# Performance work log

Hardware: AMD Instinct MI355X
Metric: run time of the kernel (lower is better)

Reference implementation:

```python
import jax, jax.numpy as jnp
import numpy as np

N = 50000      # atoms
P = 1_600_000  # pairs
F = 128        # per-atom features
G = 16         # radial basis functions
H = 32         # vector features
HID1, HID2 = 256, 128
IN_F = 2 * F + 2 * H  # is_first_module=False: [rad_emb, vec_emb, rad_q, vec_q]


def setup_inputs() -> dict:
    key = jax.random.key(0)
    ks = jax.random.split(key, 13)
    return {
        "atomic_embedding": jax.random.normal(ks[0], (N, F), jnp.float32),
        "partial_charges": jax.random.normal(ks[1], (N, 1), jnp.float32),
        "pair_indices": jax.random.randint(ks[2], (2, P), 0, N),
        "gs": jax.random.uniform(ks[3], (P, G), jnp.float32),
        "gv": jax.random.normal(ks[4], (P, 3, G), jnp.float32),
        "agh": jax.random.normal(ks[5], (F, G, H), jnp.float32) * 0.05,
        "W_gf": jax.random.normal(ks[6], (G, F), jnp.float32) * 0.1,   # gs_to_fatom (no bias)
        "W1": jax.random.normal(ks[7], (IN_F, HID1), jnp.float32) * 0.05,
        "b1": jnp.zeros((HID1,), jnp.float32),
        "W2": jax.random.normal(ks[8], (HID1, HID2), jnp.float32) * 0.05,
        "b2": jnp.zeros((HID2,), jnp.float32),
        "W3": jax.random.normal(ks[9], (HID2, F + 2), jnp.float32) * 0.05,
        "b3": jnp.zeros((F + 2,), jnp.float32),
    }


def _safe_norm(x):
    # torch.norm has subgradient 0 at 0; avoid NaN grads for all-zero rows
    sq = jnp.sum(x * x, axis=-1)
    return jnp.sqrt(jnp.where(sq > 0, sq, 1.0)) * (sq > 0)


def _gelu(x):
    return jax.nn.gelu(x, approximate=False)  # torch nn.GELU default (erf)


def reference(atomic_embedding, partial_charges, pair_indices, gs, gv, agh,
              W_gf, W1, b1, W2, b2, W3, b3):
    idx_j = pair_indices[1]                       # (P,)
    a_j = atomic_embedding[idx_j]                 # (P, F) gather
    mapped_gs = gs @ W_gf                         # (P, F)

    # radial contributions from embeddings: scatter-add over pairs
    rad_emb = jnp.zeros((N, F), mapped_gs.dtype).at[idx_j].add(a_j * mapped_gs)

    # vector contributions: einsum contraction then scatter-add, then norm
    avf_v = jnp.einsum('pa,pdg,agh->phd', a_j, gv, agh)            # (P, H, 3)
    avf_sum = jnp.zeros((N, H, 3), avf_v.dtype).at[idx_j].add(avf_v)
    vec_emb = _safe_norm(avf_sum)                                   # (N, H)

    # charge branch (vector contributions skipped -> zeros)
    q_j = partial_charges[idx_j]                                    # (P, 1)
    rad_q = jnp.zeros((N, F), mapped_gs.dtype).at[idx_j].add(q_j * mapped_gs)
    vec_q = jnp.zeros((N, H), mapped_gs.dtype)

    msg = jnp.concatenate([rad_emb, vec_emb, rad_q, vec_q], axis=1)  # (N, IN_F)
    h = _gelu(msg @ W1 + b1)
    h = _gelu(h @ W2 + b2)
    out = h @ W3 + b3                                                # (N, F+2)

    delta_q, f, delta_a = out[:, :1], out[:, 1:2], out[:, 2:]
    return (delta_a, delta_q, f)
```

## Files before the change

kernel.cpp:

```cpp
#include <hip/hip_runtime.h>
#include <math.h>

#define N_ATOMS 50000
#define P_PAIRS 1600000
#define TA 16

__device__ __forceinline__ float gelu_exact(float x) {
    return 0.5f * x * (1.0f + erff(x * 0.70710678118654752440f));
}

__global__ __launch_bounds__(256) void scatter_kernel(
    const int* __restrict__ idx_j,
    const float* __restrict__ gs,
    const float* __restrict__ gv,
    float* __restrict__ acc)
{
    int t = blockIdx.x * 256 + threadIdx.x;
    int p = t >> 6;
    int c = t & 63;
    int idx = idx_j[p];
    float v = (c < 16) ? gs[p * 16 + c] : gv[p * 48 + (c - 16)];
    atomicAdd(acc + idx * 64 + c, v);
}

__global__ __launch_bounds__(256, 2) void fused_atom_kernel(
    const float* __restrict__ emb,
    const float* __restrict__ qch,
    const float* __restrict__ acc,
    const float* __restrict__ agh,
    const float* __restrict__ W_gf,
    const float* __restrict__ W1, const float* __restrict__ b1,
    const float* __restrict__ W2, const float* __restrict__ b2,
    const float* __restrict__ W3, const float* __restrict__ b3,
    float* __restrict__ out)
{
    __shared__ __align__(16) float s_bufA[16 * 256];
    __shared__ __align__(16) float s_bufB[16 * 512];
    __shared__ __align__(16) float s_msgT[320 * 16];
    __shared__ __align__(16) float s_gs[16 * 16];
    __shared__ __align__(16) float s_gv[16 * 48];
    __shared__ __align__(16) float s_q[16];

    const int tid = threadIdx.x;
    const int n0 = blockIdx.x * TA;

    float* s_embT = s_bufA;
    float* s_U    = s_bufB;
    float* s_h1T  = s_bufA;
    float* s_h2T  = s_bufB;

    #pragma unroll
    for (int i = 0; i < 2; i++) {
        int ii = tid + i * 256;
        int atom = ii >> 5;
        int a4 = (ii & 31) * 4;
        float4 v = *(const float4*)(emb + (size_t)(n0 + atom) * 128 + a4);
        s_embT[(a4 + 0) * 16 + atom] = v.x;
        s_embT[(a4 + 1) * 16 + atom] = v.y;
        s_embT[(a4 + 2) * 16 + atom] = v.z;
        s_embT[(a4 + 3) * 16 + atom] = v.w;
    }
    #pragma unroll
    for (int i = 0; i < 4; i++) {
        int ii = tid + i * 256;
        int atom = ii >> 6, c = ii & 63;
        float v = acc[(size_t)(n0 + atom) * 64 + c];
        if (c < 16) s_gs[atom * 16 + c] = v;
        else        s_gv[atom * 48 + (c - 16)] = v;
    }
    if (tid < 16) s_q[tid] = qch[n0 + tid];
    __syncthreads();

    {
        const int gh4  = (tid & 127) * 4;
        const int half = tid >> 7;
        float u[32];
        #pragma unroll
        for (int i = 0; i < 32; i++) u[i] = 0.f;
        #pragma unroll 4
        for (int a = 0; a < 128; a++) {
            float4 w  = *(const float4*)(agh + a * 512 + gh4);
            float4 e0 = *(const float4*)(s_embT + a * 16 + half * 8);
            float4 e1 = *(const float4*)(s_embT + a * 16 + half * 8 + 4);
            float wv[4] = {w.x, w.y, w.z, w.w};
            float ev[8] = {e0.x, e0.y, e0.z, e0.w, e1.x, e1.y, e1.z, e1.w};
            #pragma unroll
            for (int j = 0; j < 4; j++)
                #pragma unroll
                for (int m = 0; m < 8; m++)
                    u[j * 8 + m] += wv[j] * ev[m];
        }
        #pragma unroll
        for (int m = 0; m < 8; m++) {
            int atom = half * 8 + m;
            float4 v = {u[0 * 8 + m], u[1 * 8 + m], u[2 * 8 + m], u[3 * 8 + m]};
            *(float4*)(s_U + atom * 512 + gh4) = v;
        }
    }
    __syncthreads();

    #pragma unroll
    for (int it = 0; it < 2; it++) {
        int i = tid + it * 256;
        int atom = i >> 5, h = i & 31;
        float v0 = 0.f, v1 = 0.f, v2 = 0.f;
        #pragma unroll
        for (int g = 0; g < 16; g++) {
            float uv = s_U[atom * 512 + g * 32 + h];
            v0 += uv * s_gv[atom * 48 + g];
            v1 += uv * s_gv[atom * 48 + 16 + g];
            v2 += uv * s_gv[atom * 48 + 32 + g];
        }
        float sq = v0 * v0 + v1 * v1 + v2 * v2;
        float nrm = (sq > 0.f) ? sqrtf(sq) : 0.f;
        s_msgT[(128 + h) * 16 + atom] = nrm;
        s_msgT[(288 + h) * 16 + atom] = 0.f;
    }

    {
        const int f = tid & 127;
        const int half = tid >> 7;
        float mp[8];
        #pragma unroll
        for (int a = 0; a < 8; a++) mp[a] = 0.f;
        #pragma unroll
        for (int g = 0; g < 16; g++) {
            float w = W_gf[g * 128 + f];
            #pragma unroll
            for (int a = 0; a < 8; a++)
                mp[a] += s_gs[(half * 8 + a) * 16 + g] * w;
        }
        #pragma unroll
        for (int a = 0; a < 8; a++) {
            int atom = half * 8 + a;
            float e = s_embT[f * 16 + atom];
            s_msgT[f * 16 + atom]         = e * mp[a];
            s_msgT[(160 + f) * 16 + atom] = s_q[atom] * mp[a];
        }
    }
    __syncthreads();

    {
        const int o4 = (tid & 63) * 4;
        const int q4 = (tid >> 6) * 4;
        float acc1[16];
        #pragma unroll
        for (int i = 0; i < 16; i++) acc1[i] = 0.f;
        #pragma unroll 4
        for (int k = 0; k < 320; k++) {
            float4 w  = *(const float4*)(W1 + k * 256 + o4);
            float4 mm = *(const float4*)(s_msgT + k * 16 + q4);
            float wv[4] = {w.x, w.y, w.z, w.w};
            float mv[4] = {mm.x, mm.y, mm.z, mm.w};
            #pragma unroll
            for (int j = 0; j < 4; j++)
                #pragma unroll
                for (int m = 0; m < 4; m++)
                    acc1[j * 4 + m] += wv[j] * mv[m];
        }
        #pragma unroll
        for (int j = 0; j < 4; j++) {
            int o = o4 + j;
            float bb = b1[o];
            float4 v;
            v.x = gelu_exact(acc1[j * 4 + 0] + bb);
            v.y = gelu_exact(acc1[j * 4 + 1] + bb);
            v.z = gelu_exact(acc1[j * 4 + 2] + bb);
            v.w = gelu_exact(acc1[j * 4 + 3] + bb);
            *(float4*)(s_h1T + o * 16 + q4) = v;
        }
    }
    __syncthreads();

    {
        const int o4 = (tid & 31) * 4;
        const int a2 = (tid >> 5) * 2;
        float acc2[8];
        #pragma unroll
        for (int i = 0; i < 8; i++) acc2[i] = 0.f;
        #pragma unroll 4
        for (int k = 0; k < 256; k++) {
            float4 w  = *(const float4*)(W2 + k * 128 + o4);
            float2 hh = *(const float2*)(s_h1T + k * 16 + a2);
            float wv[4] = {w.x, w.y, w.z, w.w};
            float hv[2] = {hh.x, hh.y};
            #pragma unroll
            for (int j = 0; j < 4; j++)
                #pragma unroll
                for (int m = 0; m < 2; m++)
                    acc2[j * 2 + m] += wv[j] * hv[m];
        }
        #pragma unroll
        for (int j = 0; j < 4; j++) {
            int o = o4 + j;
            float bb = b2[o];
            float2 v;
            v.x = gelu_exact(acc2[j * 2 + 0] + bb);
            v.y = gelu_exact(acc2[j * 2 + 1] + bb);
            *(float2*)(s_h2T + o * 16 + a2) = v;
        }
    }
    __syncthreads();

    {
        const int o4 = (tid & 31) * 4 + 2;
        const int a2 = (tid >> 5) * 2;
        float acc3[8];
        #pragma unroll
        for (int i = 0; i < 8; i++) acc3[i] = 0.f;
        #pragma unroll 4
        for (int k = 0; k < 128; k++) {
            const float* wp = W3 + k * 130 + o4;
            float2 wa = *(const float2*)(wp);
            float2 wb = *(const float2*)(wp + 2);
            float2 hh = *(const float2*)(s_h2T + k * 16 + a2);
            float wv[4] = {wa.x, wa.y, wb.x, wb.y};
            float hv[2] = {hh.x, hh.y};
            #pragma unroll
            for (int j = 0; j < 4; j++)
                #pragma unroll
                for (int m = 0; m < 2; m++)
                    acc3[j * 2 + m] += wv[j] * hv[m];
        }
        #pragma unroll
        for (int m = 0; m < 2; m++) {
            int n = n0 + a2 + m;
            float4 v;
            v.x = acc3[0 * 2 + m] + b3[o4 + 0];
            v.y = acc3[1 * 2 + m] + b3[o4 + 1];
            v.z = acc3[2 * 2 + m] + b3[o4 + 2];
            v.w = acc3[3 * 2 + m] + b3[o4 + 3];
            *(float4*)(out + (size_t)n * 128 + (o4 - 2)) = v;
        }

        if (tid < 32) {
            int atom = tid >> 1, col = tid & 1;
            float s = 0.f;
            #pragma unroll 4
            for (int k = 0; k < 128; k++)
                s += s_h2T[k * 16 + atom] * W3[k * 130 + col];
            s += b3[col];
            out[(size_t)N_ATOMS * 128 + (size_t)col * N_ATOMS + (n0 + atom)] = s;
        }
    }
}

extern "C" void kernel_launch(void* const* d_in, const int* in_sizes, int n_in,
                              void* d_out, int out_size, void* d_ws, size_t ws_size,
                              hipStream_t stream)
{
    const float* emb  = (const float*)d_in[0];
    const float* qch  = (const float*)d_in[1];
    const int*   pidx = (const int*)d_in[2];
    const float* gs   = (const float*)d_in[3];
    const float* gv   = (const float*)d_in[4];
    const float* agh  = (const float*)d_in[5];
    const float* W_gf = (const float*)d_in[6];
    const float* W1   = (const float*)d_in[7];
    const float* b1   = (const float*)d_in[8];
    const float* W2   = (const float*)d_in[9];
    const float* b2   = (const float*)d_in[10];
    const float* W3   = (const float*)d_in[11];
    const float* b3   = (const float*)d_in[12];

    float* acc = (float*)d_ws;

    hipMemsetAsync(acc, 0, (size_t)N_ATOMS * 64 * sizeof(float), stream);

    scatter_kernel<<<(P_PAIRS * 64) / 256, 256, 0, stream>>>(
        pidx + P_PAIRS, gs, gv, acc);

    fused_atom_kernel<<<N_ATOMS / TA, 256, 0, stream>>>(
        emb, qch, acc, agh, W_gf, W1, b1, W2, b2, W3, b3, (float*)d_out);
}
```

Baseline: 1.171 ms.

## Replace float atomic scatter with counting-sort segmented reduction per atom

Swaps the per-element float atomicAdd scatter of gs/gv into per-atom accumulators for a counting sort: histogram the destination indices, scan into segment offsets, scatter pair ids into sorted order, then have one wavefront per atom sum its pairs' 64 values. This removes about 100M contended float atomics and the memset of the accumulator. In exchange it adds four kernel launches, a single-block scan, integer atomics, and indirect gathers of gs/gv rows. Summation order now depends on the nondeterministic order from the scatter step.

After: 1.327 ms. 13.3% more time.

```diff
diff --git a/kernel.cpp b/kernel.cpp
--- a/kernel.cpp
+++ b/kernel.cpp
@@ -4,24 +4,114 @@
 #define N_ATOMS 50000
 #define P_PAIRS 1600000
 #define TA 16
+#define SCAN_THREADS 1024
+#define SCAN_CHUNK 49
 
 __device__ __forceinline__ float gelu_exact(float x) {
     return 0.5f * x * (1.0f + erff(x * 0.70710678118654752440f));
 }
 
-__global__ __launch_bounds__(256) void scatter_kernel(
+
+__global__ __launch_bounds__(256) void hist_kernel(
+    const int* __restrict__ idx_j, int* __restrict__ counts)
+{
+    int t = blockIdx.x * 256 + threadIdx.x;
+    if (t < P_PAIRS) atomicAdd(counts + idx_j[t], 1);
+}
+
+__global__ __launch_bounds__(SCAN_THREADS) void scan_kernel(
+    const int* __restrict__ counts,
+    int* __restrict__ seg_off,
+    int* __restrict__ cursor)
+{
+    __shared__ int s[SCAN_THREADS];
+    const int t = threadIdx.x;
+    const int base = t * SCAN_CHUNK;
+
+    int sum = 0;
+    #pragma unroll
+    for (int i = 0; i < SCAN_CHUNK; i++) {
+        int j = base + i;
+        if (j < N_ATOMS) sum += counts[j];
+    }
+    s[t] = sum;
+    __syncthreads();
+
+    #pragma unroll
+    for (int off = 1; off < SCAN_THREADS; off <<= 1) {
+        int v = 0;
+        if (t >= off) v = s[t - off];
+        __syncthreads();
+        if (t >= off) s[t] += v;
+        __syncthreads();
+    }
+
+    int run = s[t] - sum;
+    for (int i = 0; i < SCAN_CHUNK; i++) {
+        int j = base + i;
+        if (j < N_ATOMS) {
+            seg_off[j] = run;
+            cursor[j]  = run;
+            run += counts[j];
+        }
+    }
+    if (t == 0) seg_off[N_ATOMS] = P_PAIRS;
+}
+
+__global__ __launch_bounds__(256) void scatter_idx_kernel(
     const int* __restrict__ idx_j,
+    int* __restrict__ cursor,
+    int* __restrict__ sorted_p)
+{
+    int t = blockIdx.x * 256 + threadIdx.x;
+    if (t < P_PAIRS) {
+        int idx = idx_j[t];
+        int pos = atomicAdd(cursor + idx, 1);
+        sorted_p[pos] = t;
+    }
+}
+
+__global__ __launch_bounds__(256) void reduce_kernel(
+    const int* __restrict__ seg_off,
+    const int* __restrict__ sorted_p,
     const float* __restrict__ gs,
     const float* __restrict__ gv,
     float* __restrict__ acc)
 {
-    int t = blockIdx.x * 256 + threadIdx.x;
-    int p = t >> 6;
-    int c = t & 63;
-    int idx = idx_j[p];
-    float v = (c < 16) ? gs[p * 16 + c] : gv[p * 48 + (c - 16)];
-    atomicAdd(acc + idx * 64 + c, v);
-}
+    const int wave = (blockIdx.x * 256 + threadIdx.x) >> 6;
+    const int lane = threadIdx.x & 63;
+    if (wave >= N_ATOMS) return;
+
+    const int start = seg_off[wave];
+    const int end   = seg_off[wave + 1];
+    const int c = lane;
+    const bool is_gs = (c < 16);
+    const int c16 = c - 16;
+
+    float a = 0.f;
+    for (int i0 = start; i0 < end; i0 += 64) {
+        const int nb = min(64, end - i0);
+        int pl = (i0 + lane < end) ? sorted_p[i0 + lane] : 0;
+        int j = 0;
+        for (; j + 4 <= nb; j += 4) {
+            int p0 = __shfl(pl, j + 0);
+            int p1 = __shfl(pl, j + 1);
+            int p2 = __shfl(pl, j + 2);
+            int p3 = __shfl(pl, j + 3);
+            float v0 = is_gs ? gs[p0 * 16 + c] : gv[p0 * 48 + c16];
+            float v1 = is_gs ? gs[p1 * 16 + c] : gv[p1 * 48 + c16];
+            float v2 = is_gs ? gs[p2 * 16 + c] : gv[p2 * 48 + c16];
+            float v3 = is_gs ? gs[p3 * 16 + c] : gv[p3 * 48 + c16];
+            a += v0; a += v1; a += v2; a += v3;
+        }
+        for (; j < nb; j++) {
+            int p = __shfl(pl, j);
+            a += is_gs ? gs[p * 16 + c] : gv[p * 48 + c16];
+        }
+    }
+    acc[(size_t)wave * 64 + lane] = a;
+}
+
 
 __global__ __launch_bounds__(256, 2) void fused_atom_kernel(
     const float* __restrict__ emb,
@@ -262,13 +352,20 @@
     const float* b2   = (const float*)d_in[10];
     const float* W3   = (const float*)d_in[11];
     const float* b3   = (const float*)d_in[12];
-
-    float* acc = (float*)d_ws;
-
-    hipMemsetAsync(acc, 0, (size_t)N_ATOMS * 64 * sizeof(float), stream);
-
-    scatter_kernel<<<(P_PAIRS * 64) / 256, 256, 0, stream>>>(
-        pidx + P_PAIRS, gs, gv, acc);
+    const int*   idx_j = pidx + P_PAIRS;
+
+    float* acc      = (float*)d_ws;
+    int*   counts   = (int*)(acc + (size_t)N_ATOMS * 64);
+    int*   seg_off  = counts + N_ATOMS;
+    int*   cursor   = seg_off + N_ATOMS + 1;
+    int*   sorted_p = cursor + N_ATOMS;
+
+    hipMemsetAsync(counts, 0, (size_t)N_ATOMS * sizeof(int), stream);
+
+    hist_kernel<<<(P_PAIRS + 255) / 256, 256, 0, stream>>>(idx_j, counts);
+    scan_kernel<<<1, SCAN_THREADS, 0, stream>>>(counts, seg_off, cursor);
+    scatter_idx_kernel<<<(P_PAIRS + 255) / 256, 256, 0, stream>>>(idx_j, cursor, sorted_p);
+    reduce_kernel<<<(N_ATOMS + 3) / 4, 256, 0, stream>>>(seg_off, sorted_p, gs, gv, acc);
 
     fused_atom_kernel<<<N_ATOMS / TA, 256, 0, stream>>>(
         emb, qch, acc, agh, W_gf, W1, b1, W2, b2, W3, b3, (float*)d_out);
```
